# Performance work log

Hardware: AMD Instinct MI355X
Metric: run time of the kernel (lower is better)

Reference implementation:

```python
import jax, jax.numpy as jnp
import numpy as np

DIM = 1024
NUM_HEADS = 16
HEAD_DIM = 64  # DIM // NUM_HEADS
BATCH = 2
SEQ = 2048


def setup_inputs() -> dict:
    key = jax.random.key(0)
    ks = jax.random.split(key, 6)
    x = jax.random.normal(ks[0], (BATCH, SEQ, DIM), dtype=jnp.float32)
    # Linear weights stored as [in, out] so y = x @ W (same math as torch Linear).
    Wq = jax.random.normal(ks[1], (DIM, DIM), dtype=jnp.float32) * (DIM ** -0.5)
    # MQA: single shared KV head of size HEAD_DIM.
    Wk = jax.random.normal(ks[2], (DIM, HEAD_DIM), dtype=jnp.float32) * (DIM ** -0.5)
    Wv = jax.random.normal(ks[3], (DIM, HEAD_DIM), dtype=jnp.float32) * (DIM ** -0.5)
    Wo = jax.random.normal(ks[4], (DIM, DIM), dtype=jnp.float32) * (DIM ** -0.5)
    bo = jax.random.normal(ks[5], (DIM,), dtype=jnp.float32) * 0.01
    return {"x": x, "Wq": Wq, "Wk": Wk, "Wv": Wv, "Wo": Wo, "bo": bo}


def reference(x, Wq, Wk, Wv, Wo, bo):
    b, s, _ = x.shape
    scale = HEAD_DIM ** -0.5
    # Per-head queries [b, h, s, d]
    q = (x @ Wq).reshape(b, s, NUM_HEADS, HEAD_DIM).transpose(0, 2, 1, 3) * scale
    # Shared single KV head [b, s, d]
    k = x @ Wk
    v = x @ Wv
    # Materialized scores [b, h, s_q, s_k]
    scores = jnp.einsum('bhqd,bkd->bhqk', q, k)
    causal = jnp.tril(jnp.ones((s, s), dtype=bool))  # True where allowed
    scores = jnp.where(causal, scores, -jnp.inf)
    # Manual stable softmax (max, exp, sum, div) as in the original
    max_scores = jnp.max(scores, axis=-1, keepdims=True)
    exp_scores = jnp.exp(scores - max_scores)
    attn = exp_scores / jnp.sum(exp_scores, axis=-1, keepdims=True)
    out = jnp.einsum('bhqk,bkd->bhqd', attn, v)  # [b, h, s, d]
    out = out.transpose(0, 2, 1, 3).reshape(b, s, DIM)
    return out @ Wo + bo
```

## Files before the change

kernel.cpp:

```cpp
#include <hip/hip_runtime.h>

typedef unsigned short u16;
typedef __attribute__((ext_vector_type(8))) short short8;
typedef __attribute__((ext_vector_type(4))) float f32x4;

static __device__ __forceinline__ u16 f32_to_bf16(float f) {
  unsigned u = __float_as_uint(f);
  u += 0x7fffu + ((u >> 16) & 1u);
  return (u16)(u >> 16);
}

static __device__ __forceinline__ void async16(u16* lds, const u16* g) {
  __builtin_amdgcn_global_load_lds(
      (const __attribute__((address_space(1))) void*)g,
      (__attribute__((address_space(3))) void*)lds, 16, 0, 0);
}


__global__ void __launch_bounds__(256) prep_kernel(
    const float* __restrict__ x,
    const float* __restrict__ Wq, const float* __restrict__ Wk,
    const float* __restrict__ Wv, const float* __restrict__ Wo,
    u16* __restrict__ Xb, u16* __restrict__ WqT, u16* __restrict__ WkvT,
    u16* __restrict__ WoT) {
  __shared__ u16 T[64][72];
  int id = blockIdx.x;
  int tid = threadIdx.x;
  if (id < 2048) {
    int base = (id * 256 + tid) * 8;
    float4 a = *(const float4*)&x[base];
    float4 b = *(const float4*)&x[base + 4];
    short8 v;
    v[0] = (short)f32_to_bf16(a.x); v[1] = (short)f32_to_bf16(a.y);
    v[2] = (short)f32_to_bf16(a.z); v[3] = (short)f32_to_bf16(a.w);
    v[4] = (short)f32_to_bf16(b.x); v[5] = (short)f32_to_bf16(b.y);
    v[6] = (short)f32_to_bf16(b.z); v[7] = (short)f32_to_bf16(b.w);
    *(short8*)&Xb[base] = v;
    return;
  }
  int id2 = id - 2048;
  const float* src; u16* dst; int tk, tn, src_ld, row_off;
  if (id2 < 256)      { src = Wq; dst = WqT;  tk = id2 & 15; tn = id2 >> 4; src_ld = 1024; row_off = 0; }
  else if (id2 < 512) { int i = id2 - 256; src = Wo; dst = WoT; tk = i & 15; tn = i >> 4; src_ld = 1024; row_off = 0; }
  else if (id2 < 528) { src = Wk; dst = WkvT; tk = id2 - 512; tn = 0; src_ld = 64; row_off = 0; }
  else                { src = Wv; dst = WkvT; tk = id2 - 528; tn = 0; src_ld = 64; row_off = 64; }
  int k0 = tk * 64, n0 = tn * 64;
#pragma unroll
  for (int it = 0; it < 2; ++it) {
    int c = tid + it * 256;
    int r = c >> 3, cc = (c & 7) * 8;
    const float* p = &src[(k0 + r) * src_ld + n0 + cc];
    float4 a = *(const float4*)&p[0];
    float4 b = *(const float4*)&p[4];
    short8 v;
    v[0] = (short)f32_to_bf16(a.x); v[1] = (short)f32_to_bf16(a.y);
    v[2] = (short)f32_to_bf16(a.z); v[3] = (short)f32_to_bf16(a.w);
    v[4] = (short)f32_to_bf16(b.x); v[5] = (short)f32_to_bf16(b.y);
    v[6] = (short)f32_to_bf16(b.z); v[7] = (short)f32_to_bf16(b.w);
    *(short8*)&T[r][cc] = v;
  }
  __syncthreads();
#pragma unroll
  for (int it = 0; it < 2; ++it) {
    int c = tid + it * 256;
    int r = c >> 3, cc = (c & 7) * 8;
    short8 v;
#pragma unroll
    for (int j = 0; j < 8; ++j) v[j] = (short)T[cc + j][r];
    *(short8*)&dst[(row_off + n0 + r) * 1024 + k0 + cc] = v;
  }
}

__device__ __forceinline__ void stage_64x128(
    const u16* __restrict__ A, const u16* __restrict__ BT, int m0, int K,
    int k0, u16* As, u16* Bs, int w, int lrow, int swz8) {
#pragma unroll
  for (int it = 0; it < 2; ++it) {
    int W = w * 2 + it;
    async16(As + W * 512, &A[(size_t)(m0 + W * 8 + lrow) * K + k0 + swz8]);
  }
#pragma unroll
  for (int it = 0; it < 4; ++it) {
    int W = w * 4 + it;
    async16(Bs + W * 512, &BT[(size_t)(W * 8 + lrow) * K + k0 + swz8]);
  }
}

__device__ __forceinline__ void gemm_core_64x128_db(
    const u16* __restrict__ A, const u16* __restrict__ BT, int m0, int K,
    f32x4 (&acc)[2][4], u16* As, u16* Bs,
    int lane, int w, int wr, int wc, int g, int lo) {
  int lrow = lane >> 3;
  int swz8 = ((lane & 7) ^ lrow) * 8;
  int lo7 = lo & 7;
  const int NK = K >> 6;
  stage_64x128(A, BT, m0, K, 0, As, Bs, w, lrow, swz8);
  for (int kt = 0; kt < NK; ++kt) {
    int cur = kt & 1;
    __syncthreads();
    if (kt + 1 < NK)
      stage_64x128(A, BT, m0, K, (kt + 1) * 64,
                   As + (cur ^ 1) * 4096, Bs + (cur ^ 1) * 8192, w, lrow, swz8);
    const u16* Asc = As + cur * 4096;
    const u16* Bsc = Bs + cur * 8192;
#pragma unroll
    for (int ks = 0; ks < 2; ++ks) {
      int pc = ((ks * 4 + g) ^ lo7) * 8;
      short8 af[2], bf[4];
#pragma unroll
      for (int i = 0; i < 2; ++i)
        af[i] = *(const short8*)&Asc[(wr * 32 + i * 16 + lo) * 64 + pc];
#pragma unroll
      for (int i = 0; i < 4; ++i)
        bf[i] = *(const short8*)&Bsc[(wc * 64 + i * 16 + lo) * 64 + pc];
#pragma unroll
      for (int mi = 0; mi < 2; ++mi)
#pragma unroll
        for (int ni = 0; ni < 4; ++ni)
          acc[mi][ni] = __builtin_amdgcn_mfma_f32_16x16x32_bf16(
              af[mi], bf[ni], acc[mi][ni], 0, 0, 0);
    }
  }
}

__global__ void __launch_bounds__(256) qkv_gemm(
    const u16* __restrict__ Xb, const u16* __restrict__ WqT,
    const u16* __restrict__ WkvT, u16* __restrict__ Qb, u16* __restrict__ KVb,
    u16* __restrict__ VTb) {
  __shared__ u16 As[2 * 64 * 64];
  __shared__ u16 Bs[2 * 128 * 64];
  int tid = threadIdx.x, lane = tid & 63, w = tid >> 6;
  int wr = w >> 1, wc = w & 1, g = lane >> 4, lo = lane & 15;
  int m0 = blockIdx.x * 64, nb = blockIdx.y;
  const u16* BT = (nb < 8) ? (WqT + (size_t)nb * 128 * 1024) : WkvT;
  f32x4 acc[2][4];
  f32x4 zz = {0.f, 0.f, 0.f, 0.f};
#pragma unroll
  for (int i = 0; i < 2; ++i)
#pragma unroll
    for (int j = 0; j < 4; ++j) acc[i][j] = zz;
  gemm_core_64x128_db(Xb, BT, m0, 1024, acc, As, Bs, lane, w, wr, wc, g, lo);
#pragma unroll
  for (int mi = 0; mi < 2; ++mi)
#pragma unroll
    for (int ni = 0; ni < 4; ++ni)
#pragma unroll
      for (int r = 0; r < 4; ++r) {
        int row = m0 + wr * 32 + mi * 16 + g * 4 + r;
        int col = wc * 64 + ni * 16 + lo;
        u16 v = f32_to_bf16(acc[mi][ni][r]);
        if (nb < 8) {
          Qb[row * 1024 + nb * 128 + col] = v;
        } else if (wc == 0) {
          KVb[row * 64 + col] = v;
        } else {
          int d = col - 64;
          VTb[(((row >> 11) * 64) + d) * 2048 + (row & 2047)] = v;
        }
      }
}

__global__ void __launch_bounds__(256, 2) attn_kernel(
    const u16* __restrict__ Qb, const u16* __restrict__ KVb,
    const u16* __restrict__ VTb, u16* __restrict__ AOb) {
  __shared__ u16 Ks[2][64 * 64];
  __shared__ u16 Vt[2][64 * 64];
  __shared__ u16 Ps[4][16][72];
  int tid = threadIdx.x, lane = tid & 63, w = tid >> 6;
  int gq = lane >> 4, lo = lane & 15;
  int pg = blockIdx.x;
  int h = blockIdx.y;
  int z = blockIdx.z;
  int b = z;
  int a = z ? (15 - pg) : pg;
  int hi = 31 - a;
  int qb_lo = a * 64 + w * 16;
  int qb_hi = hi * 64 + w * 16;
  int lrow = lane >> 3;
  int swz8 = ((lane & 7) ^ lrow) * 8;
  int lo7 = lo & 7;

  short8 qf_lo[2], qf_hi[2];
  {
    const u16* qp = &Qb[(size_t)(b * 2048 + qb_lo + lo) * 1024 + h * 64];
    qf_lo[0] = *(const short8*)&qp[gq * 8];
    qf_lo[1] = *(const short8*)&qp[32 + gq * 8];
    const u16* qp2 = &Qb[(size_t)(b * 2048 + qb_hi + lo) * 1024 + h * 64];
    qf_hi[0] = *(const short8*)&qp2[gq * 8];
    qf_hi[1] = *(const short8*)&qp2[32 + gq * 8];
  }

  short8 ones;
#pragma unroll
  for (int j = 0; j < 8; ++j) ones[j] = (short)0x3F80;

  f32x4 zz = {0.f, 0.f, 0.f, 0.f};
  f32x4 oacc_lo[4], oacc_hi[4], l_lo, l_hi;
#pragma unroll
  for (int i = 0; i < 4; ++i) { oacc_lo[i] = zz; oacc_hi[i] = zz; }
  l_lo = zz; l_hi = zz;

  const float kExp = 0.18033688011112042f;
  const float kOff = 11.541560327111707f;

  auto do_strip = [&](const short8 (&qf)[2], f32x4 (&oacc)[4], f32x4& l_acc,
                      int qbase, bool diag, int k0,
                      const u16* Kc, const u16* Vc) {
    f32x4 sacc[4];
#pragma unroll
    for (int ns = 0; ns < 4; ++ns) sacc[ns] = zz;
#pragma unroll
    for (int ks = 0; ks < 2; ++ks) {
      int pc = ((ks * 4 + gq) ^ lo7) * 8;
      short8 kf[4];
#pragma unroll
      for (int ns = 0; ns < 4; ++ns)
        kf[ns] = *(const short8*)&Kc[(ns * 16 + lo) * 64 + pc];
#pragma unroll
      for (int ns = 0; ns < 4; ++ns)
        sacc[ns] = __builtin_amdgcn_mfma_f32_16x16x32_bf16(
            qf[ks], kf[ns], sacc[ns], 0, 0, 0);
    }
#pragma unroll
    for (int ns = 0; ns < 4; ++ns)
#pragma unroll
      for (int r = 0; r < 4; ++r) {
        float p = __builtin_amdgcn_exp2f(fmaf(sacc[ns][r], kExp, -kOff));
        if (diag) {
          int qg = qbase + gq * 4 + r;
          int kg = k0 + ns * 16 + lo;
          if (kg > qg) p = 0.f;
        }
        Ps[w][gq * 4 + r][ns * 16 + lo] = (u16)(__float_as_uint(p) >> 16);
      }
    __threadfence_block();
#pragma unroll
    for (int k2 = 0; k2 < 2; ++k2) {
      short8 pf = *(const short8*)&Ps[w][lo][k2 * 32 + gq * 8];
      int pc = ((k2 * 4 + gq) ^ lo7) * 8;
      short8 vf[4];
#pragma unroll
      for (int ds = 0; ds < 4; ++ds)
        vf[ds] = *(const short8*)&Vc[(ds * 16 + lo) * 64 + pc];
#pragma unroll
      for (int ds = 0; ds < 4; ++ds)
        oacc[ds] = __builtin_amdgcn_mfma_f32_16x16x32_bf16(
            pf, vf[ds], oacc[ds], 0, 0, 0);
      l_acc = __builtin_amdgcn_mfma_f32_16x16x32_bf16(pf, ones, l_acc, 0, 0, 0);
    }
  };

  auto stage_kv = [&](int t, int bu) {
#pragma unroll
    for (int it = 0; it < 2; ++it) {
      int W = w * 2 + it;
      async16(&Ks[bu][W * 512],
              &KVb[(size_t)(b * 2048 + t * 64 + W * 8 + lrow) * 64 + swz8]);
      async16(&Vt[bu][W * 512],
              &VTb[((size_t)b * 64 + W * 8 + lrow) * 2048 + t * 64 + swz8]);
    }
  };

  int nst = hi + 1;
  stage_kv(0, 0);
  for (int t = 0; t < nst; ++t) {
    int cur = t & 1;
    __syncthreads();
    if (t + 1 < nst) stage_kv(t + 1, cur ^ 1);
    int k0 = t * 64;
    do_strip(qf_hi, oacc_hi, l_hi, qb_hi, t == hi, k0, Ks[cur], Vt[cur]);
    if (t <= a)
      do_strip(qf_lo, oacc_lo, l_lo, qb_lo, t == a, k0, Ks[cur], Vt[cur]);
  }

#pragma unroll
  for (int r = 0; r < 4; ++r) {
    float inv_lo = 1.0f / l_lo[r];
    float inv_hi = 1.0f / l_hi[r];
    int row_lo = b * 2048 + qb_lo + gq * 4 + r;
    int row_hi = b * 2048 + qb_hi + gq * 4 + r;
#pragma unroll
    for (int ds = 0; ds < 4; ++ds) {
      AOb[row_lo * 1024 + h * 64 + ds * 16 + lo] = f32_to_bf16(oacc_lo[ds][r] * inv_lo);
      AOb[row_hi * 1024 + h * 64 + ds * 16 + lo] = f32_to_bf16(oacc_hi[ds][r] * inv_hi);
    }
  }
}

__global__ void __launch_bounds__(256) out_gemm(
    const u16* __restrict__ A, const u16* __restrict__ WoT,
    const float* __restrict__ bias, float* __restrict__ C) {
  __shared__ u16 As[2 * 64 * 64];
  __shared__ u16 Bs[2 * 128 * 64];
  int tid = threadIdx.x, lane = tid & 63, w = tid >> 6;
  int wr = w >> 1, wc = w & 1, g = lane >> 4, lo = lane & 15;
  int m0 = blockIdx.x * 64, nb = blockIdx.y;
  const u16* BT = WoT + (size_t)nb * 128 * 1024;
  f32x4 acc[2][4];
  f32x4 zz = {0.f, 0.f, 0.f, 0.f};
#pragma unroll
  for (int i = 0; i < 2; ++i)
#pragma unroll
    for (int j = 0; j < 4; ++j) acc[i][j] = zz;
  gemm_core_64x128_db(A, BT, m0, 1024, acc, As, Bs, lane, w, wr, wc, g, lo);
#pragma unroll
  for (int mi = 0; mi < 2; ++mi)
#pragma unroll
    for (int ni = 0; ni < 4; ++ni)
#pragma unroll
      for (int r = 0; r < 4; ++r) {
        int row = m0 + wr * 32 + mi * 16 + g * 4 + r;
        int col = nb * 128 + wc * 64 + ni * 16 + lo;
        C[row * 1024 + col] = acc[mi][ni][r] + bias[col];
      }
}

extern "C" void kernel_launch(void* const* d_in, const int* in_sizes, int n_in,
                              void* d_out, int out_size, void* d_ws, size_t ws_size,
                              hipStream_t stream) {
  const float* x  = (const float*)d_in[0];
  const float* Wq = (const float*)d_in[1];
  const float* Wk = (const float*)d_in[2];
  const float* Wv = (const float*)d_in[3];
  const float* Wo = (const float*)d_in[4];
  const float* bo = (const float*)d_in[5];
  float* out = (float*)d_out;

  u16* ws   = (u16*)d_ws;
  u16* AOb  = ws;
  u16* KVb  = AOb + 4194304;
  u16* VTb  = KVb + 262144;
  u16* Xb   = VTb + 262144;
  u16* WqT  = Xb + 4194304;
  u16* WoT  = WqT + 1048576;
  u16* WkvT = WoT + 1048576;
  u16* Qb   = (u16*)d_out;

  prep_kernel<<<2592, 256, 0, stream>>>(x, Wq, Wk, Wv, Wo, Xb, WqT, WkvT, WoT);
  qkv_gemm<<<dim3(64, 9), 256, 0, stream>>>(Xb, WqT, WkvT, Qb, KVb, VTb);
  attn_kernel<<<dim3(16, 16, 2), 256, 0, stream>>>(Qb, KVb, VTb, AOb);
  out_gemm<<<dim3(64, 8), 256, 0, stream>>>(AOb, WoT, bo, out);
}
```

Measured before the change: 156.4 us.

## Restructure attention to 512-thread blocks over contiguous 128-row query tiles

Replaces the paired lo/hi query-strip scheme, where each 4-wave block handled two 64-row strips for causal balance, with 8-wave blocks that each own one contiguous 128-row query tile. Every wave processes a single 16-row strip. The K/V tile staging is now spread across 8 waves, one async load each instead of two. Per-block causal work is no longer balanced, though the batch index still reverses tile order. Waves whose rows end before a given key tile still compute that tile and rely on masking, which wastes some work, and the diag mask test is broader.

```diff
diff --git a/kernel.cpp b/kernel.cpp
--- a/kernel.cpp
+++ b/kernel.cpp
@@ -160,34 +160,30 @@
       }
 }
 
-__global__ void __launch_bounds__(256, 2) attn_kernel(
+__global__ void __launch_bounds__(512) attn_kernel(
     const u16* __restrict__ Qb, const u16* __restrict__ KVb,
     const u16* __restrict__ VTb, u16* __restrict__ AOb) {
   __shared__ u16 Ks[2][64 * 64];
   __shared__ u16 Vt[2][64 * 64];
-  __shared__ u16 Ps[4][16][72];
+  __shared__ u16 Ps[8][16][72];
   int tid = threadIdx.x, lane = tid & 63, w = tid >> 6;
   int gq = lane >> 4, lo = lane & 15;
-  int pg = blockIdx.x;
-  int h = blockIdx.y;
+  int h = blockIdx.x;
+  int by = blockIdx.y;
   int z = blockIdx.z;
   int b = z;
-  int a = z ? (15 - pg) : pg;
-  int hi = 31 - a;
-  int qb_lo = a * 64 + w * 16;
-  int qb_hi = hi * 64 + w * 16;
+  int qt = z ? (15 - by) : by;
+  int q0 = qt * 128;
+  int qbase = q0 + w * 16;
   int lrow = lane >> 3;
   int swz8 = ((lane & 7) ^ lrow) * 8;
   int lo7 = lo & 7;
 
-  short8 qf_lo[2], qf_hi[2];
+  short8 qf[2];
   {
-    const u16* qp = &Qb[(size_t)(b * 2048 + qb_lo + lo) * 1024 + h * 64];
-    qf_lo[0] = *(const short8*)&qp[gq * 8];
-    qf_lo[1] = *(const short8*)&qp[32 + gq * 8];
-    const u16* qp2 = &Qb[(size_t)(b * 2048 + qb_hi + lo) * 1024 + h * 64];
-    qf_hi[0] = *(const short8*)&qp2[gq * 8];
-    qf_hi[1] = *(const short8*)&qp2[32 + gq * 8];
+    const u16* qp = &Qb[(size_t)(b * 2048 + qbase + lo) * 1024 + h * 64];
+    qf[0] = *(const short8*)&qp[gq * 8];
+    qf[1] = *(const short8*)&qp[32 + gq * 8];
   }
 
   short8 ones;
@@ -195,17 +191,29 @@
   for (int j = 0; j < 8; ++j) ones[j] = (short)0x3F80;
 
   f32x4 zz = {0.f, 0.f, 0.f, 0.f};
-  f32x4 oacc_lo[4], oacc_hi[4], l_lo, l_hi;
-#pragma unroll
-  for (int i = 0; i < 4; ++i) { oacc_lo[i] = zz; oacc_hi[i] = zz; }
-  l_lo = zz; l_hi = zz;
+  f32x4 oacc[4], l_acc;
+#pragma unroll
+  for (int i = 0; i < 4; ++i) oacc[i] = zz;
+  l_acc = zz;
 
   const float kExp = 0.18033688011112042f;
   const float kOff = 11.541560327111707f;
 
-  auto do_strip = [&](const short8 (&qf)[2], f32x4 (&oacc)[4], f32x4& l_acc,
-                      int qbase, bool diag, int k0,
-                      const u16* Kc, const u16* Vc) {
+  auto stage_kv = [&](int t, int bu) {
+    async16(&Ks[bu][w * 512],
+            &KVb[(size_t)(b * 2048 + t * 64 + w * 8 + lrow) * 64 + swz8]);
+    async16(&Vt[bu][w * 512],
+            &VTb[((size_t)b * 64 + w * 8 + lrow) * 2048 + t * 64 + swz8]);
+  };
+
+  int nst = 2 * qt + 2;
+  stage_kv(0, 0);
+  for (int t = 0; t < nst; ++t) {
+    int cur = t & 1;
+    __syncthreads();
+    if (t + 1 < nst) stage_kv(t + 1, cur ^ 1);
+    int k0 = t * 64;
+
     f32x4 sacc[4];
 #pragma unroll
     for (int ns = 0; ns < 4; ++ns) sacc[ns] = zz;
@@ -215,12 +223,14 @@
       short8 kf[4];
 #pragma unroll
       for (int ns = 0; ns < 4; ++ns)
-        kf[ns] = *(const short8*)&Kc[(ns * 16 + lo) * 64 + pc];
+        kf[ns] = *(const short8*)&Ks[cur][(ns * 16 + lo) * 64 + pc];
 #pragma unroll
       for (int ns = 0; ns < 4; ++ns)
         sacc[ns] = __builtin_amdgcn_mfma_f32_16x16x32_bf16(
             qf[ks], kf[ns], sacc[ns], 0, 0, 0);
     }
+
+    bool diag = (k0 + 63) > qbase;
 #pragma unroll
     for (int ns = 0; ns < 4; ++ns)
 #pragma unroll
@@ -234,6 +244,7 @@
         Ps[w][gq * 4 + r][ns * 16 + lo] = (u16)(__float_as_uint(p) >> 16);
       }
     __threadfence_block();
+
 #pragma unroll
     for (int k2 = 0; k2 < 2; ++k2) {
       short8 pf = *(const short8*)&Ps[w][lo][k2 * 32 + gq * 8];
@@ -241,49 +252,22 @@
       short8 vf[4];
 #pragma unroll
       for (int ds = 0; ds < 4; ++ds)
-        vf[ds] = *(const short8*)&Vc[(ds * 16 + lo) * 64 + pc];
+        vf[ds] = *(const short8*)&Vt[cur][(ds * 16 + lo) * 64 + pc];
 #pragma unroll
       for (int ds = 0; ds < 4; ++ds)
         oacc[ds] = __builtin_amdgcn_mfma_f32_16x16x32_bf16(
             pf, vf[ds], oacc[ds], 0, 0, 0);
       l_acc = __builtin_amdgcn_mfma_f32_16x16x32_bf16(pf, ones, l_acc, 0, 0, 0);
     }
-  };
-
-  auto stage_kv = [&](int t, int bu) {
-#pragma unroll
-    for (int it = 0; it < 2; ++it) {
-      int W = w * 2 + it;
-      async16(&Ks[bu][W * 512],
-              &KVb[(size_t)(b * 2048 + t * 64 + W * 8 + lrow) * 64 + swz8]);
-      async16(&Vt[bu][W * 512],
-              &VTb[((size_t)b * 64 + W * 8 + lrow) * 2048 + t * 64 + swz8]);
-    }
-  };
-
-  int nst = hi + 1;
-  stage_kv(0, 0);
-  for (int t = 0; t < nst; ++t) {
-    int cur = t & 1;
-    __syncthreads();
-    if (t + 1 < nst) stage_kv(t + 1, cur ^ 1);
-    int k0 = t * 64;
-    do_strip(qf_hi, oacc_hi, l_hi, qb_hi, t == hi, k0, Ks[cur], Vt[cur]);
-    if (t <= a)
-      do_strip(qf_lo, oacc_lo, l_lo, qb_lo, t == a, k0, Ks[cur], Vt[cur]);
   }
 
 #pragma unroll
   for (int r = 0; r < 4; ++r) {
-    float inv_lo = 1.0f / l_lo[r];
-    float inv_hi = 1.0f / l_hi[r];
-    int row_lo = b * 2048 + qb_lo + gq * 4 + r;
-    int row_hi = b * 2048 + qb_hi + gq * 4 + r;
-#pragma unroll
-    for (int ds = 0; ds < 4; ++ds) {
-      AOb[row_lo * 1024 + h * 64 + ds * 16 + lo] = f32_to_bf16(oacc_lo[ds][r] * inv_lo);
-      AOb[row_hi * 1024 + h * 64 + ds * 16 + lo] = f32_to_bf16(oacc_hi[ds][r] * inv_hi);
-    }
+    float inv_l = 1.0f / l_acc[r];
+    int row = b * 2048 + qbase + gq * 4 + r;
+#pragma unroll
+    for (int ds = 0; ds < 4; ++ds)
+      AOb[row * 1024 + h * 64 + ds * 16 + lo] = f32_to_bf16(oacc[ds][r] * inv_l);
   }
 }
 
@@ -338,6 +322,6 @@
 
   prep_kernel<<<2592, 256, 0, stream>>>(x, Wq, Wk, Wv, Wo, Xb, WqT, WkvT, WoT);
   qkv_gemm<<<dim3(64, 9), 256, 0, stream>>>(Xb, WqT, WkvT, Qb, KVb, VTb);
-  attn_kernel<<<dim3(16, 16, 2), 256, 0, stream>>>(Qb, KVb, VTb, AOb);
+  attn_kernel<<<dim3(16, 16, 2), 512, 0, stream>>>(Qb, KVb, VTb, AOb);
   out_gemm<<<dim3(64, 8), 256, 0, stream>>>(AOb, WoT, bo, out);
 }
```

Result: slower. 164.0 us (+4.9%).
